# Performance work log

Hardware: AMD Instinct MI355X
Metric: run time of the kernel (lower is better)

## Reference

```python
import jax, jax.numpy as jnp
import numpy as np

B, S, HID = 2, 2048, 2048
NH, NKV, D = 16, 8, 128
EPS = 1e-6
THETA = 10000.0


def _rms_norm(x, w):
    # RMSNorm over last dim (head_dim), Qwen3-style per-head q/k norm
    var = jnp.mean(jnp.square(x), axis=-1, keepdims=True)
    return x * jax.lax.rsqrt(var + EPS) * w


def _rotate_half(x):
    x1, x2 = jnp.split(x, 2, axis=-1)
    return jnp.concatenate([-x2, x1], axis=-1)


def setup_inputs() -> dict:
    key = jax.random.key(0)
    ks = jax.random.split(key, 8)
    hidden_states = jax.random.normal(ks[0], (B, S, HID), dtype=jnp.float32)
    # rotary embeddings (HF-style: emb = concat(freqs, freqs))
    inv_freq = 1.0 / (THETA ** (jnp.arange(0, D, 2, dtype=jnp.float32) / D))
    pos = jnp.arange(S, dtype=jnp.float32)
    freqs = jnp.outer(pos, inv_freq)                      # [S, D/2]
    emb = jnp.concatenate([freqs, freqs], axis=-1)        # [S, D]
    cos = jnp.broadcast_to(jnp.cos(emb)[None], (B, S, D))
    sin = jnp.broadcast_to(jnp.sin(emb)[None], (B, S, D))
    w_scale = 1.0 / np.sqrt(HID)
    Wq = jax.random.normal(ks[1], (HID, NH * D), dtype=jnp.float32) * w_scale
    Wk = jax.random.normal(ks[2], (HID, NKV * D), dtype=jnp.float32) * w_scale
    Wv = jax.random.normal(ks[3], (HID, NKV * D), dtype=jnp.float32) * w_scale
    Wo = jax.random.normal(ks[4], (NH * D, HID), dtype=jnp.float32) * w_scale
    q_norm_w = jnp.ones((D,), dtype=jnp.float32)
    k_norm_w = jnp.ones((D,), dtype=jnp.float32)
    return {"hidden_states": hidden_states, "cos": cos, "sin": sin,
            "Wq": Wq, "Wk": Wk, "Wv": Wv, "Wo": Wo,
            "q_norm_w": q_norm_w, "k_norm_w": k_norm_w}


def reference(hidden_states, cos, sin, Wq, Wk, Wv, Wo, q_norm_w, k_norm_w):
    b, s, _ = hidden_states.shape
    # projections + per-head RMSNorm on q/k, then [B,H,S,D]
    q = _rms_norm((hidden_states @ Wq).reshape(b, s, NH, D), q_norm_w)
    k = _rms_norm((hidden_states @ Wk).reshape(b, s, NKV, D), k_norm_w)
    v = (hidden_states @ Wv).reshape(b, s, NKV, D)
    q = jnp.swapaxes(q, 1, 2)  # [B,NH,S,D]
    k = jnp.swapaxes(k, 1, 2)  # [B,NKV,S,D]
    v = jnp.swapaxes(v, 1, 2)
    # rotary position embedding
    c = cos[:, None, :, :]
    sn = sin[:, None, :, :]
    q = q * c + _rotate_half(q) * sn
    k = k * c + _rotate_half(k) * sn
    # GQA: expand kv heads to match query heads
    rep = NH // NKV
    k = jnp.repeat(k, rep, axis=1)
    v = jnp.repeat(v, rep, axis=1)
    # scaled causal attention (splash_attention semantics, causal mask)
    q = q * (D ** -0.5)
    scores = jnp.einsum('bhqd,bhkd->bhqk', q, k)
    causal = jnp.tril(jnp.ones((s, s), dtype=bool))
    scores = jnp.where(causal[None, None], scores, jnp.finfo(scores.dtype).min)
    attn = jax.nn.softmax(scores, axis=-1)
    out = jnp.einsum('bhqk,bhkd->bhqd', attn, v)
    out = jnp.swapaxes(out, 1, 2).reshape(b, s, NH * D)
    return out @ Wo
```

## Files before the change

kernel.cpp:

```cpp
#include <hip/hip_runtime.h>
#include <hip/hip_bf16.h>

typedef unsigned short u16;
typedef unsigned int u32;
typedef unsigned long long u64;
typedef __attribute__((ext_vector_type(8))) short short8;
typedef __attribute__((ext_vector_type(4))) float floatx4;

#define AS1 __attribute__((address_space(1)))
#define AS3 __attribute__((address_space(3)))

__device__ __forceinline__ float bf2f(u16 u) {
    u32 x = ((u32)u) << 16;
    float f;
    __builtin_memcpy(&f, &x, 4);
    return f;
}
__device__ __forceinline__ u16 f2bf(float f) {
    u32 x;
    __builtin_memcpy(&x, &f, 4);
    u32 r = (x + 0x7fffu + ((x >> 16) & 1u)) >> 16;
    return (u16)r;
}
__device__ __forceinline__ u32 f2bf_pk(float a, float b) {
    __hip_bfloat162 h = __float22bfloat162_rn(float2{a, b});
    u32 r;
    __builtin_memcpy(&r, &h, 4);
    return r;
}

__global__ __launch_bounds__(256) void prep_weights(const float* __restrict__ Wq,
                                                    const float* __restrict__ Wk,
                                                    const float* __restrict__ Wv,
                                                    const float* __restrict__ Wo,
                                                    const float* __restrict__ X,
                                                    u16* __restrict__ WqkvT,
                                                    u16* __restrict__ WoT,
                                                    u16* __restrict__ Xb) {
    const int z = blockIdx.z;
    const int tx = threadIdx.x, ty = threadIdx.y;
    if (z == 4) {
        int tid = ty * 32 + tx;
        int idx = blockIdx.y * 32 + blockIdx.x;
        if (idx >= 1024) return;
        size_t base = (size_t)idx * 256 + tid;
#pragma unroll
        for (int p = 0; p < 8; p++) {
            size_t i = (base + (size_t)p * 262144) * 4;
            float4 v = *(const float4*)(X + i);
            u16 o[4] = {f2bf(v.x), f2bf(v.y), f2bf(v.z), f2bf(v.w)};
            *(u64*)(Xb + i) = *(u64*)o;
        }
        return;
    }
    const float* in;
    u16* out;
    int C;
    if (z == 0) { in = Wq; out = WqkvT; C = 2048; }
    else if (z == 1) { in = Wk; out = WqkvT + 2048 * 2048; C = 1024; }
    else if (z == 2) { in = Wv; out = WqkvT + 3072 * 2048; C = 1024; }
    else { in = Wo; out = WoT; C = 2048; }
    const int c0 = blockIdx.x * 64, r0 = blockIdx.y * 64;
    if (c0 >= C) return;
    __shared__ u16 t[64][66];
#pragma unroll
    for (int p = 0; p < 4; p++) {
        int rr = (ty + 8 * p) * 2;
#pragma unroll
        for (int i = 0; i < 2; i++) {
            float2 v = *(const float2*)(in + (size_t)(r0 + rr + i) * C + c0 + tx * 2);
            *(u32*)&t[rr + i][tx * 2] = f2bf_pk(v.x, v.y);
        }
    }
    __syncthreads();
#pragma unroll
    for (int p = 0; p < 4; p++) {
        int cc = (ty + 8 * p) * 2;
        u32 a = *(const u32*)&t[tx * 2][cc];
        u32 bq = *(const u32*)&t[tx * 2 + 1][cc];
        u32 pk0 = (a & 0xffffu) | (bq << 16);
        u32 pk1 = (a >> 16) | (bq & 0xffff0000u);
        *(u32*)(out + (size_t)(c0 + cc) * 2048 + r0 + tx * 2) = pk0;
        *(u32*)(out + (size_t)(c0 + cc + 1) * 2048 + r0 + tx * 2) = pk1;
    }
}

template <typename OUT_T, bool FUSEV>
__global__ __launch_bounds__(512, 2) void gemm256(const u16* __restrict__ A,
                                                  const u16* __restrict__ Bt,
                                                  OUT_T* __restrict__ C,
                                                  u16* __restrict__ Vt,
                                                  int M, int N, int K) {
    (void)M;
    __shared__ __align__(16) u16 lds[2][2][2][128 * 64];
    const int tid = threadIdx.x;
    const int wave = tid >> 6, lane = tid & 63;
    const int lr = lane & 15, lq = lane >> 4;
    const int wm = wave >> 2, wn = wave & 3;
    const int m0 = blockIdx.y * 256, n0 = blockIdx.x * 256;

    const int srow = lane >> 3;
    const int schunk = ((lane & 7) ^ srow) << 3;
    const int slot = wave << 1;

    auto stage = [&](const u16* src, int rbase, int buf, int mat, int half, int k0) {
#pragma unroll
        for (int j = 0; j < 2; j++) {
            int r = rbase + half * 128 + (slot + j) * 8 + srow;
            __builtin_amdgcn_global_load_lds(
                (const AS1 void*)(src + (size_t)r * K + k0 + schunk),
                (AS3 void*)(&lds[buf][mat][half][(slot + j) * 512]), 16, 0, 0);
        }
    };

    floatx4 zf = {0.f, 0.f, 0.f, 0.f};
    floatx4 acc[8][4];
#pragma unroll
    for (int i = 0; i < 8; i++)
#pragma unroll
        for (int jn = 0; jn < 4; jn++) acc[i][jn] = zf;

    const int NT = K >> 6;

    stage(Bt, n0, 0, 1, 0, 0);
    stage(Bt, n0, 0, 1, 1, 0);
    stage(A, m0, 0, 0, 0, 0);
    stage(A, m0, 0, 0, 1, 0);
    if (NT > 1) {
        stage(Bt, n0, 1, 1, 0, 64);
        stage(Bt, n0, 1, 1, 1, 64);
        stage(A, m0, 1, 0, 0, 64);
        asm volatile("s_waitcnt vmcnt(6)" ::: "memory");
    } else {
        asm volatile("s_waitcnt vmcnt(0)" ::: "memory");
    }
    __builtin_amdgcn_s_barrier();

    for (int kt = 0; kt < NT; kt++) {
        const int b = kt & 1;
        const u16* Ab = &lds[b][0][wm][0];
        const u16* Bb = &lds[b][1][wn >> 1][0];
        const int brow = (wn & 1) * 64;
        const int sx = lr & 7;
        const int nk = (kt + 2) << 6;

        short8 bf0[4], bf1[4], af[4];
#pragma unroll
        for (int jn = 0; jn < 4; jn++) {
            int rh = brow + jn * 16 + lr;
            bf0[jn] = *(const short8*)(Bb + rh * 64 + ((lq ^ sx) << 3));
            bf1[jn] = *(const short8*)(Bb + rh * 64 + (((4 + lq) ^ sx) << 3));
        }
#pragma unroll
        for (int i = 0; i < 4; i++)
            af[i] = *(const short8*)(Ab + (i * 16 + lr) * 64 + ((lq ^ sx) << 3));
        if (kt + 1 < NT) stage(A, m0, b ^ 1, 0, 1, (kt + 1) << 6);
        __builtin_amdgcn_s_barrier();
        asm volatile("s_waitcnt lgkmcnt(0)" ::: "memory");
        __builtin_amdgcn_sched_barrier(0);
        __builtin_amdgcn_s_setprio(1);
#pragma unroll
        for (int i = 0; i < 4; i++)
#pragma unroll
            for (int jn = 0; jn < 4; jn++)
                acc[i][jn] = __builtin_amdgcn_mfma_f32_16x16x32_bf16(af[i], bf0[jn], acc[i][jn], 0, 0, 0);
        __builtin_amdgcn_s_setprio(0);
        __builtin_amdgcn_s_barrier();

        short8 ag[4];
#pragma unroll
        for (int i = 0; i < 4; i++)
            ag[i] = *(const short8*)(Ab + ((i + 4) * 16 + lr) * 64 + ((lq ^ sx) << 3));
        if (kt + 2 < NT) stage(Bt, n0, b, 1, 0, nk);
        __builtin_amdgcn_s_barrier();
        asm volatile("s_waitcnt lgkmcnt(0)" ::: "memory");
        __builtin_amdgcn_sched_barrier(0);
        __builtin_amdgcn_s_setprio(1);
#pragma unroll
        for (int i = 0; i < 4; i++)
#pragma unroll
            for (int jn = 0; jn < 4; jn++)
                acc[i + 4][jn] = __builtin_amdgcn_mfma_f32_16x16x32_bf16(ag[i], bf0[jn], acc[i + 4][jn], 0, 0, 0);
        __builtin_amdgcn_s_setprio(0);
        __builtin_amdgcn_s_barrier();

        short8 c0[4], c1[4];
#pragma unroll
        for (int i = 0; i < 4; i++) {
            c0[i] = *(const short8*)(Ab + (i * 16 + lr) * 64 + (((4 + lq) ^ sx) << 3));
            c1[i] = *(const short8*)(Ab + ((i + 4) * 16 + lr) * 64 + (((4 + lq) ^ sx) << 3));
        }
        if (kt + 2 < NT) stage(Bt, n0, b, 1, 1, nk);
        __builtin_amdgcn_s_barrier();
        asm volatile("s_waitcnt lgkmcnt(0)" ::: "memory");
        __builtin_amdgcn_sched_barrier(0);
        __builtin_amdgcn_s_setprio(1);
#pragma unroll
        for (int i = 0; i < 4; i++)
#pragma unroll
            for (int jn = 0; jn < 4; jn++)
                acc[i][jn] = __builtin_amdgcn_mfma_f32_16x16x32_bf16(c0[i], bf1[jn], acc[i][jn], 0, 0, 0);
        __builtin_amdgcn_s_setprio(0);
        __builtin_amdgcn_s_barrier();

        if (kt + 2 < NT) stage(A, m0, b, 0, 0, nk);
        __builtin_amdgcn_s_barrier();
        __builtin_amdgcn_s_setprio(1);
#pragma unroll
        for (int i = 0; i < 4; i++)
#pragma unroll
            for (int jn = 0; jn < 4; jn++)
                acc[i + 4][jn] = __builtin_amdgcn_mfma_f32_16x16x32_bf16(c1[i], bf1[jn], acc[i + 4][jn], 0, 0, 0);
        __builtin_amdgcn_s_setprio(0);
        if (kt + 2 < NT) asm volatile("s_waitcnt vmcnt(6)" ::: "memory");
        else asm volatile("s_waitcnt vmcnt(0)" ::: "memory");
        __builtin_amdgcn_s_barrier();
    }

    if (FUSEV && n0 >= 3072) {
        const int bb = m0 >> 11;
        const int sbase = (m0 & 2047) + wm * 128 + lq * 4;
#pragma unroll
        for (int i = 0; i < 8; i++)
#pragma unroll
            for (int jn = 0; jn < 4; jn++) {
                int dcol = (n0 - 3072) + wn * 64 + jn * 16 + lr;
                int kv = dcol >> 7, d = dcol & 127;
                u16 o[4] = {f2bf(acc[i][jn][0]), f2bf(acc[i][jn][1]),
                            f2bf(acc[i][jn][2]), f2bf(acc[i][jn][3])};
                *(u64*)(Vt + (size_t)((bb * 8 + kv) * 128 + d) * 2048 +
                        sbase + i * 16) = *(u64*)o;
            }
        return;
    }

#pragma unroll
    for (int i = 0; i < 8; i++)
#pragma unroll
        for (int jn = 0; jn < 4; jn++)
#pragma unroll
            for (int r = 0; r < 4; r++) {
                int row = m0 + wm * 128 + i * 16 + lq * 4 + r;
                int col = n0 + wn * 64 + jn * 16 + lr;
                if constexpr (sizeof(OUT_T) == 2)
                    C[(size_t)row * N + col] = f2bf(acc[i][jn][r]);
                else
                    C[(size_t)row * N + col] = acc[i][jn][r];
            }
}

template <typename OUT_T>
__global__ __launch_bounds__(512, 2) void gemm128n(const u16* __restrict__ A,
                                                   const u16* __restrict__ Bt,
                                                   OUT_T* __restrict__ C,
                                                   int M, int N, int K) {
    (void)M;
    __shared__ __align__(16) u16 Abuf[2][2][128 * 64];
    __shared__ __align__(16) u16 Bbuf[2][128 * 64];
    const int tid = threadIdx.x;
    const int wave = tid >> 6, lane = tid & 63;
    const int lr = lane & 15, lq = lane >> 4;
    const int wm = wave >> 1, wn = wave & 1;
    const int m0 = blockIdx.y * 256, n0 = blockIdx.x * 128;

    const int srow = lane >> 3;
    const int schunk = ((lane & 7) ^ srow) << 3;
    const int slot = wave << 1;

    auto stage = [&](const u16* src, int rowbase, u16* ldsbase, int k0) {
#pragma unroll
        for (int j = 0; j < 2; j++) {
            int r = rowbase + (slot + j) * 8 + srow;
            __builtin_amdgcn_global_load_lds(
                (const AS1 void*)(src + (size_t)r * K + k0 + schunk),
                (AS3 void*)(ldsbase + (slot + j) * 512), 16, 0, 0);
        }
    };

    floatx4 zf = {0.f, 0.f, 0.f, 0.f};
    floatx4 acc[4][4];
#pragma unroll
    for (int i = 0; i < 4; i++)
#pragma unroll
        for (int jn = 0; jn < 4; jn++) acc[i][jn] = zf;

    const int NT = K >> 6;

    stage(A, m0, &Abuf[0][0][0], 0);
    stage(A, m0 + 128, &Abuf[0][1][0], 0);
    stage(Bt, n0, &Bbuf[0][0], 0);
    if (NT > 1) {
        stage(A, m0, &Abuf[1][0][0], 64);
        stage(Bt, n0, &Bbuf[1][0], 64);
        asm volatile("s_waitcnt vmcnt(4)" ::: "memory");
    } else {
        asm volatile("s_waitcnt vmcnt(0)" ::: "memory");
    }
    __builtin_amdgcn_s_barrier();

    for (int kt = 0; kt < NT; kt++) {
        const int b = kt & 1;
        const u16* Ab = &Abuf[b][wm >> 1][0];
        const u16* Bb = &Bbuf[b][0];
        const int ar = (wm & 1) * 64;
        const int br = wn * 64;
        const int sx = lr & 7;
        const int nk = (kt + 2) << 6;

        short8 bf0[4], bf1[4], af[4];
#pragma unroll
        for (int jn = 0; jn < 4; jn++) {
            int rh = br + jn * 16 + lr;
            bf0[jn] = *(const short8*)(Bb + rh * 64 + ((lq ^ sx) << 3));
            bf1[jn] = *(const short8*)(Bb + rh * 64 + (((4 + lq) ^ sx) << 3));
        }
#pragma unroll
        for (int i = 0; i < 4; i++)
            af[i] = *(const short8*)(Ab + (ar + i * 16 + lr) * 64 + ((lq ^ sx) << 3));
        if (kt + 1 < NT) stage(A, m0 + 128, &Abuf[b ^ 1][1][0], (kt + 1) << 6);
        __builtin_amdgcn_s_barrier();
        asm volatile("s_waitcnt lgkmcnt(0)" ::: "memory");
        __builtin_amdgcn_sched_barrier(0);
        __builtin_amdgcn_s_setprio(1);
#pragma unroll
        for (int i = 0; i < 2; i++)
#pragma unroll
            for (int jn = 0; jn < 4; jn++)
                acc[i][jn] = __builtin_amdgcn_mfma_f32_16x16x32_bf16(af[i], bf0[jn], acc[i][jn], 0, 0, 0);
        __builtin_amdgcn_s_setprio(0);
        __builtin_amdgcn_s_barrier();

        if (kt + 2 < NT) stage(Bt, n0, &Bbuf[b][0], nk);
        __builtin_amdgcn_s_barrier();
        __builtin_amdgcn_s_setprio(1);
#pragma unroll
        for (int i = 2; i < 4; i++)
#pragma unroll
            for (int jn = 0; jn < 4; jn++)
                acc[i][jn] = __builtin_amdgcn_mfma_f32_16x16x32_bf16(af[i], bf0[jn], acc[i][jn], 0, 0, 0);
        __builtin_amdgcn_s_setprio(0);
        __builtin_amdgcn_s_barrier();

        short8 ag[4];
#pragma unroll
        for (int i = 0; i < 4; i++)
            ag[i] = *(const short8*)(Ab + (ar + i * 16 + lr) * 64 + (((4 + lq) ^ sx) << 3));
        __builtin_amdgcn_s_barrier();
        asm volatile("s_waitcnt lgkmcnt(0)" ::: "memory");
        __builtin_amdgcn_sched_barrier(0);
        __builtin_amdgcn_s_setprio(1);
#pragma unroll
        for (int i = 0; i < 2; i++)
#pragma unroll
            for (int jn = 0; jn < 4; jn++)
                acc[i][jn] = __builtin_amdgcn_mfma_f32_16x16x32_bf16(ag[i], bf1[jn], acc[i][jn], 0, 0, 0);
        __builtin_amdgcn_s_setprio(0);
        __builtin_amdgcn_s_barrier();

        if (kt + 2 < NT) stage(A, m0, &Abuf[b][0][0], nk);
        __builtin_amdgcn_s_barrier();
        __builtin_amdgcn_s_setprio(1);
#pragma unroll
        for (int i = 2; i < 4; i++)
#pragma unroll
            for (int jn = 0; jn < 4; jn++)
                acc[i][jn] = __builtin_amdgcn_mfma_f32_16x16x32_bf16(ag[i], bf1[jn], acc[i][jn], 0, 0, 0);
        __builtin_amdgcn_s_setprio(0);
        if (kt + 2 < NT) asm volatile("s_waitcnt vmcnt(4)" ::: "memory");
        else asm volatile("s_waitcnt vmcnt(0)" ::: "memory");
        __builtin_amdgcn_s_barrier();
    }

#pragma unroll
    for (int i = 0; i < 4; i++)
#pragma unroll
        for (int jn = 0; jn < 4; jn++)
#pragma unroll
            for (int r = 0; r < 4; r++) {
                int row = m0 + wm * 64 + i * 16 + lq * 4 + r;
                int col = n0 + wn * 64 + jn * 16 + lr;
                if constexpr (sizeof(OUT_T) == 2)
                    C[(size_t)row * N + col] = f2bf(acc[i][jn][r]);
                else
                    C[(size_t)row * N + col] = acc[i][jn][r];
            }
}

__global__ __launch_bounds__(256) void prep_qkv(u16* __restrict__ QKV,
                                                const float* __restrict__ cosb,
                                                const float* __restrict__ sinb,
                                                const float* __restrict__ qw,
                                                const float* __restrict__ kw) {
    const int bx = blockIdx.x;
    const int tid = threadIdx.x;
    const int wave = tid >> 6, lane = tid & 63;
    const int half = lane >> 5, l5 = lane & 31;
    const int t = bx * 4 + wave;
    const int R = t * 2 + half;
    u16* ptr;
    const float* w;
    float scale;
    int bs;
    if (R < 65536) {
        bs = R >> 4;
        ptr = QKV + (size_t)bs * 4096 + (R & 15) * 128;
        w = qw;
        scale = 0.08838834764831845f * 1.4426950408889634f;
    } else {
        int R2 = R - 65536;
        bs = R2 >> 3;
        ptr = QKV + (size_t)bs * 4096 + 2048 + (R2 & 7) * 128;
        w = kw;
        scale = 1.0f;
    }
    const int d = l5 * 4;
    u64 xv = *(const u64*)(ptr + d);
    float x0 = bf2f((u16)xv), x1 = bf2f((u16)(xv >> 16));
    float x2 = bf2f((u16)(xv >> 32)), x3 = bf2f((u16)(xv >> 48));
    float ss = x0 * x0 + x1 * x1 + x2 * x2 + x3 * x3;
#pragma unroll
    for (int off = 1; off < 32; off <<= 1) ss += __shfl_xor(ss, off);
    float rn = rsqrtf(ss * (1.0f / 128.0f) + 1e-6f);
    float4 wv = *(const float4*)(w + d);
    float y0 = x0 * rn * wv.x, y1 = x1 * rn * wv.y;
    float y2 = x2 * rn * wv.z, y3 = x3 * rn * wv.w;
    float p0 = __shfl_xor(y0, 16), p1 = __shfl_xor(y1, 16);
    float p2 = __shfl_xor(y2, 16), p3 = __shfl_xor(y3, 16);
    float sgn = (l5 < 16) ? -1.0f : 1.0f;
    float4 cv = *(const float4*)(cosb + (size_t)bs * 128 + d);
    float4 sv = *(const float4*)(sinb + (size_t)bs * 128 + d);
    float o0 = (y0 * cv.x + sgn * p0 * sv.x) * scale;
    float o1 = (y1 * cv.y + sgn * p1 * sv.y) * scale;
    float o2 = (y2 * cv.z + sgn * p2 * sv.z) * scale;
    float o3 = (y3 * cv.w + sgn * p3 * sv.w) * scale;
    u64 res = (u64)f2bf_pk(o0, o1) | ((u64)f2bf_pk(o2, o3) << 32);
    *(u64*)(ptr + d) = res;
}

__global__ __launch_bounds__(256, 3) void attn_kernel(const u16* __restrict__ QKV,
                                                      const u16* __restrict__ Vt,
                                                      u16* __restrict__ O) {
    __shared__ __align__(16) u16 Ks[2][16 * 520];
    __shared__ __align__(16) u16 Vs[18 * 520];
    const int tid = threadIdx.x;
    const int wave = tid >> 6, lane = tid & 63;
    const int lr = lane & 15, lq = lane >> 4;

    const int id = blockIdx.x;
    const int qt = 31 - (id >> 5);
    const int j = id & 31;
    const int h = j & 15;
    const int b = j >> 4;

    const int kv = h >> 1;
    const int q0 = qt * 64;
    const int wq = wave * 16;

    auto stageK = [&](int buf, int k0s) {
#pragma unroll
        for (int jj = 0; jj < 4; jj++) {
            int r = wave * 16 + jj * 4 + (lane >> 4);
            int ch = (lane & 15) ^ (r & 15);
            __builtin_amdgcn_global_load_lds(
                (const AS1 void*)(QKV + (size_t)(b * 2048 + k0s + r) * 4096 + 2048 + kv * 128 + ch * 8),
                (AS3 void*)(&Ks[buf][(wave * 4 + jj) * 520]), 16, 0, 0);
        }
    };
    auto stageV = [&](int k0s) {
#pragma unroll
        for (int jj = 0; jj < 4; jj++) {
            int r = wave * 32 + jj * 8 + (lane >> 3);
            int ch = (lane & 7) ^ (r & 7);
            __builtin_amdgcn_global_load_lds(
                (const AS1 void*)(Vt + (size_t)((b * 8 + kv) * 128 + r) * 2048 + k0s + ch * 8),
                (AS3 void*)(&Vs[(wave * 4 + jj) * 520]), 16, 0, 0);
        }
    };

#pragma unroll
    for (int k = tid; k < 260; k += 256)
        *(u64*)(&Vs[8320 + k * 4]) = 0x3F803F803F803F80ULL;
    asm volatile("s_waitcnt lgkmcnt(0)" ::: "memory");

    short8 qf[4];
#pragma unroll
    for (int t = 0; t < 4; t++)
        qf[t] = *(const short8*)(QKV + (size_t)(b * 2048 + q0 + wq + lr) * 4096 + h * 128 + t * 32 + lq * 8);

    floatx4 zf = {0.f, 0.f, 0.f, 0.f};
    floatx4 oacc[9];
#pragma unroll
    for (int jn = 0; jn < 9; jn++) oacc[jn] = zf;
    float mstate = -1e30f;

    const int nIter = qt + 1;

    stageK(0, 0);

    for (int kt = 0; kt < nIter; kt++) {
        const int k0 = kt * 64;
        const int cur = kt & 1;
        asm volatile("s_waitcnt vmcnt(0)" ::: "memory");
        __builtin_amdgcn_s_barrier();
        stageV(k0);
        if (kt + 1 < nIter) stageK(cur ^ 1, k0 + 64);

        const bool active = (k0 <= q0 + wq + 15);
        u64 pb[4];
        if (active) {
            const u16* KsC = &Ks[cur][0];
            floatx4 sacc[4];
#pragma unroll
            for (int jm = 0; jm < 4; jm++) sacc[jm] = zf;
            __builtin_amdgcn_s_setprio(1);
#pragma unroll
            for (int t = 0; t < 4; t++) {
                short8 a[4];
#pragma unroll
                for (int jm = 0; jm < 4; jm++) {
                    int off = (jm * 4 + (lr >> 2)) * 520 + (lr & 3) * 128 +
                              (((t * 4 + lq) ^ lr) << 3);
                    a[jm] = *(const short8*)(KsC + off);
                }
#pragma unroll
                for (int jm = 0; jm < 4; jm++)
                    sacc[jm] = __builtin_amdgcn_mfma_f32_16x16x32_bf16(a[jm], qf[t], sacc[jm], 0, 0, 0);
            }
            __builtin_amdgcn_s_setprio(0);

            if (k0 + 63 > q0 + wq) {
#pragma unroll
                for (int jm = 0; jm < 4; jm++) {
                    int diff = (q0 + wq + lr) - (k0 + jm * 16 + lq * 4);
#pragma unroll
                    for (int r = 0; r < 4; r++)
                        if (r > diff) sacc[jm][r] = -1e30f;
                }
            }

            float mx = -1e30f;
#pragma unroll
            for (int jm = 0; jm < 4; jm++) {
                float a0 = fmaxf(sacc[jm][0], sacc[jm][1]);
                float a1 = fmaxf(sacc[jm][2], sacc[jm][3]);
                mx = fmaxf(mx, fmaxf(a0, a1));
            }
            mx = fmaxf(mx, __shfl_xor(mx, 16));
            mx = fmaxf(mx, __shfl_xor(mx, 32));

            bool defer = __all(mx - mstate <= 8.0f);
            float mnew = defer ? mstate : fmaxf(mstate, mx);

#pragma unroll
            for (int jm = 0; jm < 4; jm++)
#pragma unroll
                for (int r = 0; r < 4; r++)
                    sacc[jm][r] = exp2f(sacc[jm][r] - mnew);

            if (!defer) {
                float alpha = exp2f(mstate - mnew);
                mstate = mnew;
                float ao[4];
#pragma unroll
                for (int r = 0; r < 4; r++) ao[r] = __shfl(alpha, lq * 4 + r);
#pragma unroll
                for (int jn = 0; jn < 9; jn++)
#pragma unroll
                    for (int r = 0; r < 4; r++) oacc[jn][r] *= ao[r];
            }

#pragma unroll
            for (int jm = 0; jm < 4; jm++) {
                u32 lo = f2bf_pk(sacc[jm][0], sacc[jm][1]);
                u32 hi = f2bf_pk(sacc[jm][2], sacc[jm][3]);
                pb[jm] = (u64)lo | ((u64)hi << 32);
            }
        }

        if (kt + 1 < nIter) asm volatile("s_waitcnt vmcnt(4)" ::: "memory");
        else                asm volatile("s_waitcnt vmcnt(0)" ::: "memory");
        __builtin_amdgcn_s_barrier();

        if (active) {
            __builtin_amdgcn_s_setprio(1);
#pragma unroll
            for (int t = 0; t < 2; t++) {
                union { short8 v; u64 q[2]; } pa;
                pa.q[0] = pb[2 * t];
                pa.q[1] = pb[2 * t + 1];
#pragma unroll
                for (int jn = 0; jn < 9; jn++) {
                    const u16* vrow = Vs + (jn * 2 + (lr >> 3)) * 520 +
                                      (lr & 7) * 64 + (lq & 1) * 4;
                    union { short8 v; u64 q[2]; } vb;
                    vb.q[0] = *(const u64*)(vrow + (((t * 4 + (lq >> 1)) ^ (lr & 7)) << 3));
                    vb.q[1] = *(const u64*)(vrow + (((t * 4 + 2 + (lq >> 1)) ^ (lr & 7)) << 3));
                    oacc[jn] = __builtin_amdgcn_mfma_f32_16x16x32_bf16(pa.v, vb.v, oacc[jn], 0, 0, 0);
                }
            }
            __builtin_amdgcn_s_setprio(0);
        }
    }

#pragma unroll
    for (int jn = 0; jn < 8; jn++)
#pragma unroll
        for (int r = 0; r < 4; r++) {
            int row = q0 + wq + lq * 4 + r;
            O[(size_t)(b * 2048 + row) * 2048 + h * 128 + jn * 16 + lr] =
                f2bf(oacc[jn][r] / oacc[8][r]);
        }
}

extern "C" void kernel_launch(void* const* d_in, const int* in_sizes, int n_in,
                              void* d_out, int out_size, void* d_ws, size_t ws_size,
                              hipStream_t stream) {
    const float* X = (const float*)d_in[0];
    const float* cosb = (const float*)d_in[1];
    const float* sinb = (const float*)d_in[2];
    const float* Wq = (const float*)d_in[3];
    const float* Wk = (const float*)d_in[4];
    const float* Wv = (const float*)d_in[5];
    const float* Wo = (const float*)d_in[6];
    const float* qw = (const float*)d_in[7];
    const float* kw = (const float*)d_in[8];
    float* out = (float*)d_out;
    u16* ws = (u16*)d_ws;

    u16* WqkvT = ws;
    u16* WoT = WqkvT + 8388608;
    u16* Xb = WoT + 4194304;
    u16* QKVb = Xb + 8388608;
    u16* Vtb = QKVb + 16777216;
    u16* Ob = Xb;

    prep_weights<<<dim3(32, 32, 5), dim3(32, 8), 0, stream>>>(Wq, Wk, Wv, Wo, X,
                                                              WqkvT, WoT, Xb);

    gemm256<u16, true><<<dim3(16, 16), 512, 0, stream>>>(Xb, WqkvT, QKVb, Vtb,
                                                         4096, 4096, 2048);

    prep_qkv<<<12288, 256, 0, stream>>>(QKVb, cosb, sinb, qw, kw);

    attn_kernel<<<1024, 256, 0, stream>>>(QKVb, Vtb, Ob);

    gemm128n<float><<<dim3(16, 16), 512, 0, stream>>>(Ob, WoT, out, 4096, 2048, 2048);
}
```

Baseline: 330.3 us.

## Fuse Q RMSNorm+RoPE into attention and remap GEMM blocks per XCD

The Q-side RMSNorm, rotary embedding and softmax scale move from the standalone prep_qkv kernel into the attention kernel's Q-fragment load, computed in registers. prep_qkv now handles only K rows, so it launches a third as many blocks and one full read-modify-write pass over Q is gone. Separately, both GEMMs use a 1D grid with an XCD-aware swizzle, so blocks placed on the same XCD cover a compact tile region for better L2 reuse. In exchange, each attention block redoes the Q normalisation and reads cos/sin itself, which adds some work to its prologue.

```diff
diff --git a/kernel.cpp b/kernel.cpp
--- a/kernel.cpp
+++ b/kernel.cpp
@@ -97,7 +97,11 @@
     const int wave = tid >> 6, lane = tid & 63;
     const int lr = lane & 15, lq = lane >> 4;
     const int wm = wave >> 2, wn = wave & 3;
-    const int m0 = blockIdx.y * 256, n0 = blockIdx.x * 256;
+    const int id = blockIdx.x;
+    const int xcd = id & 7, kk2 = id >> 3;
+    const int bx = (xcd & 3) * 4 + (kk2 & 3);
+    const int by = (xcd >> 2) * 8 + (kk2 >> 2);
+    const int m0 = by * 256, n0 = bx * 256;
 
     const int srow = lane >> 3;
     const int schunk = ((lane & 7) ^ srow) << 3;
@@ -261,7 +265,11 @@
     const int wave = tid >> 6, lane = tid & 63;
     const int lr = lane & 15, lq = lane >> 4;
     const int wm = wave >> 1, wn = wave & 1;
-    const int m0 = blockIdx.y * 256, n0 = blockIdx.x * 128;
+    const int id = blockIdx.x;
+    const int xcd = id & 7, kk2 = id >> 3;
+    const int bx = (xcd & 3) * 4 + (kk2 & 3);
+    const int by = (xcd >> 2) * 8 + (kk2 >> 2);
+    const int m0 = by * 256, n0 = bx * 128;
 
     const int srow = lane >> 3;
     const int schunk = ((lane & 7) ^ srow) << 3;
@@ -389,7 +397,6 @@
 __global__ __launch_bounds__(256) void prep_qkv(u16* __restrict__ QKV,
                                                 const float* __restrict__ cosb,
                                                 const float* __restrict__ sinb,
-                                                const float* __restrict__ qw,
                                                 const float* __restrict__ kw) {
     const int bx = blockIdx.x;
     const int tid = threadIdx.x;
@@ -397,22 +404,8 @@
     const int half = lane >> 5, l5 = lane & 31;
     const int t = bx * 4 + wave;
     const int R = t * 2 + half;
-    u16* ptr;
-    const float* w;
-    float scale;
-    int bs;
-    if (R < 65536) {
-        bs = R >> 4;
-        ptr = QKV + (size_t)bs * 4096 + (R & 15) * 128;
-        w = qw;
-        scale = 0.08838834764831845f * 1.4426950408889634f;
-    } else {
-        int R2 = R - 65536;
-        bs = R2 >> 3;
-        ptr = QKV + (size_t)bs * 4096 + 2048 + (R2 & 7) * 128;
-        w = kw;
-        scale = 1.0f;
-    }
+    const int bs = R >> 3;
+    u16* ptr = QKV + (size_t)bs * 4096 + 2048 + (R & 7) * 128;
     const int d = l5 * 4;
     u64 xv = *(const u64*)(ptr + d);
     float x0 = bf2f((u16)xv), x1 = bf2f((u16)(xv >> 16));
@@ -421,7 +414,7 @@
 #pragma unroll
     for (int off = 1; off < 32; off <<= 1) ss += __shfl_xor(ss, off);
     float rn = rsqrtf(ss * (1.0f / 128.0f) + 1e-6f);
-    float4 wv = *(const float4*)(w + d);
+    float4 wv = *(const float4*)(kw + d);
     float y0 = x0 * rn * wv.x, y1 = x1 * rn * wv.y;
     float y2 = x2 * rn * wv.z, y3 = x3 * rn * wv.w;
     float p0 = __shfl_xor(y0, 16), p1 = __shfl_xor(y1, 16);
@@ -429,17 +422,20 @@
     float sgn = (l5 < 16) ? -1.0f : 1.0f;
     float4 cv = *(const float4*)(cosb + (size_t)bs * 128 + d);
     float4 sv = *(const float4*)(sinb + (size_t)bs * 128 + d);
-    float o0 = (y0 * cv.x + sgn * p0 * sv.x) * scale;
-    float o1 = (y1 * cv.y + sgn * p1 * sv.y) * scale;
-    float o2 = (y2 * cv.z + sgn * p2 * sv.z) * scale;
-    float o3 = (y3 * cv.w + sgn * p3 * sv.w) * scale;
+    float o0 = y0 * cv.x + sgn * p0 * sv.x;
+    float o1 = y1 * cv.y + sgn * p1 * sv.y;
+    float o2 = y2 * cv.z + sgn * p2 * sv.z;
+    float o3 = y3 * cv.w + sgn * p3 * sv.w;
     u64 res = (u64)f2bf_pk(o0, o1) | ((u64)f2bf_pk(o2, o3) << 32);
     *(u64*)(ptr + d) = res;
 }
 
 __global__ __launch_bounds__(256, 3) void attn_kernel(const u16* __restrict__ QKV,
                                                       const u16* __restrict__ Vt,
-                                                      u16* __restrict__ O) {
+                                                      u16* __restrict__ O,
+                                                      const float* __restrict__ cosb,
+                                                      const float* __restrict__ sinb,
+                                                      const float* __restrict__ qw) {
     __shared__ __align__(16) u16 Ks[2][16 * 520];
     __shared__ __align__(16) u16 Vs[18 * 520];
     const int tid = threadIdx.x;
@@ -482,10 +478,61 @@
         *(u64*)(&Vs[8320 + k * 4]) = 0x3F803F803F803F80ULL;
     asm volatile("s_waitcnt lgkmcnt(0)" ::: "memory");
 
+    const int qrow_s = q0 + wq + lr;
+    const u16* qrow = QKV + (size_t)(b * 2048 + qrow_s) * 4096 + h * 128;
+    float yv[4][8];
+    float ss = 0.f;
+#pragma unroll
+    for (int t = 0; t < 4; t++) {
+        int d0 = t * 32 + lq * 8;
+        u64 v0 = *(const u64*)(qrow + d0);
+        u64 v1 = *(const u64*)(qrow + d0 + 4);
+#pragma unroll
+        for (int e = 0; e < 4; e++) {
+            yv[t][e] = bf2f((u16)(v0 >> (16 * e)));
+            yv[t][e + 4] = bf2f((u16)(v1 >> (16 * e)));
+        }
+#pragma unroll
+        for (int e = 0; e < 8; e++) ss += yv[t][e] * yv[t][e];
+    }
+    ss += __shfl_xor(ss, 16);
+    ss += __shfl_xor(ss, 32);
+    {
+        float rn = rsqrtf(ss * (1.0f / 128.0f) + 1e-6f);
+#pragma unroll
+        for (int t = 0; t < 4; t++) {
+            int d0 = t * 32 + lq * 8;
+            float4 w0 = *(const float4*)(qw + d0);
+            float4 w1 = *(const float4*)(qw + d0 + 4);
+            yv[t][0] *= rn * w0.x; yv[t][1] *= rn * w0.y;
+            yv[t][2] *= rn * w0.z; yv[t][3] *= rn * w0.w;
+            yv[t][4] *= rn * w1.x; yv[t][5] *= rn * w1.y;
+            yv[t][6] *= rn * w1.z; yv[t][7] *= rn * w1.w;
+        }
+    }
+    const float QS = 0.08838834764831845f * 1.4426950408889634f;
     short8 qf[4];
 #pragma unroll
-    for (int t = 0; t < 4; t++)
-        qf[t] = *(const short8*)(QKV + (size_t)(b * 2048 + q0 + wq + lr) * 4096 + h * 128 + t * 32 + lq * 8);
+    for (int t = 0; t < 4; t++) {
+        int d0 = t * 32 + lq * 8;
+        const float* cb = cosb + ((size_t)b * 2048 + qrow_s) * 128 + d0;
+        const float* sb = sinb + ((size_t)b * 2048 + qrow_s) * 128 + d0;
+        float4 c0 = *(const float4*)cb, c1 = *(const float4*)(cb + 4);
+        float4 s0 = *(const float4*)sb, s1 = *(const float4*)(sb + 4);
+        float sgn = (t < 2) ? -1.0f : 1.0f;
+        float o0 = (yv[t][0] * c0.x + sgn * yv[t ^ 2][0] * s0.x) * QS;
+        float o1 = (yv[t][1] * c0.y + sgn * yv[t ^ 2][1] * s0.y) * QS;
+        float o2 = (yv[t][2] * c0.z + sgn * yv[t ^ 2][2] * s0.z) * QS;
+        float o3 = (yv[t][3] * c0.w + sgn * yv[t ^ 2][3] * s0.w) * QS;
+        float o4 = (yv[t][4] * c1.x + sgn * yv[t ^ 2][4] * s1.x) * QS;
+        float o5 = (yv[t][5] * c1.y + sgn * yv[t ^ 2][5] * s1.y) * QS;
+        float o6 = (yv[t][6] * c1.z + sgn * yv[t ^ 2][6] * s1.z) * QS;
+        float o7 = (yv[t][7] * c1.w + sgn * yv[t ^ 2][7] * s1.w) * QS;
+        union { short8 v; u32 w[4]; } qq;
+        qq.w[0] = f2bf_pk(o0, o1); qq.w[1] = f2bf_pk(o2, o3);
+        qq.w[2] = f2bf_pk(o4, o5); qq.w[3] = f2bf_pk(o6, o7);
+        qf[t] = qq.v;
+    }
 
     floatx4 zf = {0.f, 0.f, 0.f, 0.f};
     floatx4 oacc[9];
@@ -637,12 +684,12 @@
     prep_weights<<<dim3(32, 32, 5), dim3(32, 8), 0, stream>>>(Wq, Wk, Wv, Wo, X,
                                                               WqkvT, WoT, Xb);
 
-    gemm256<u16, true><<<dim3(16, 16), 512, 0, stream>>>(Xb, WqkvT, QKVb, Vtb,
-                                                         4096, 4096, 2048);
-
-    prep_qkv<<<12288, 256, 0, stream>>>(QKVb, cosb, sinb, qw, kw);
-
-    attn_kernel<<<1024, 256, 0, stream>>>(QKVb, Vtb, Ob);
-
-    gemm128n<float><<<dim3(16, 16), 512, 0, stream>>>(Ob, WoT, out, 4096, 2048, 2048);
-}
+    gemm256<u16, true><<<256, 512, 0, stream>>>(Xb, WqkvT, QKVb, Vtb,
+                                                4096, 4096, 2048);
+
+    prep_qkv<<<4096, 256, 0, stream>>>(QKVb, cosb, sinb, kw);
+
+    attn_kernel<<<1024, 256, 0, stream>>>(QKVb, Vtb, Ob, cosb, sinb, qw);
+
+    gemm128n<float><<<256, 512, 0, stream>>>(Ob, WoT, out, 4096, 2048, 2048);
+}
```

Result: no change. 330.0 us (median of 2 runs) (-0.1%).
